# Kernel tuning notes

Hardware: AMD Instinct MI355X
Metric: run time of the kernel (lower is better)

The kernel has to match this reference:

```python
import jax, jax.numpy as jnp
import numpy as np

NB, H = 4, 16
EPS = 1e-5


def _ln(x, w=None, b=None):
    m = jnp.mean(x, -1, keepdims=True)
    v = jnp.var(x, -1, keepdims=True)
    y = (x - m) * jax.lax.rsqrt(v + EPS)
    if w is not None:
        y = y * w
    if b is not None:
        y = y + b
    return y


def _ada_ln(a, s, ln_s_w, w_gamma, w_beta):
    # AF3 Algorithm 26: a <- sigmoid(Lin(LN_nobias(s))) * LN_noaffine(a) + Lin(LN_nobias(s))
    a_n = _ln(a)
    s_n = _ln(s, ln_s_w)
    return jax.nn.sigmoid(s_n @ w_gamma) * a_n + s_n @ w_beta


def setup_inputs():
    key = jax.random.key(0)
    B, S, c_a, c_s, c_z = 1, 1024, 768, 384, 128
    n_hidden = 2 * c_a  # expansion factor n=2
    ks = iter(jax.random.split(key, 40))

    def rn(shape, scale=1.0):
        return scale * jax.random.normal(next(ks), shape, dtype=jnp.float32)

    p = 0.02
    return {
        "a": rn((B, S, c_a)),
        "s": rn((B, S, c_s)),
        "z": rn((B, S, S, c_z)),
        "beta": rn((B, S, S, H)),
        # per-block AttentionPairBias params (stacked over NB blocks)
        "ln_s_w_attn": jnp.ones((NB, c_s)),
        "wg_attn": rn((NB, c_s, c_a), p),
        "wb_attn": rn((NB, c_s, c_a), p),
        "wq": rn((NB, c_a, c_a), p),
        "bq": jnp.zeros((NB, c_a)),
        "wk": rn((NB, c_a, c_a), p),
        "wv": rn((NB, c_a, c_a), p),
        "ln_z_w": jnp.ones((NB, c_z)),
        "ln_z_b": jnp.zeros((NB, c_z)),
        "wpb": rn((NB, c_z, H), p),
        "wgate": rn((NB, c_a, c_a), p),
        "wo": rn((NB, c_a, c_a), p),
        "wsg_attn": rn((NB, c_s, c_a), p),
        "bsg_attn": -2.0 * jnp.ones((NB, c_a)),
        # per-block ConditionedTransitionBlock params
        "ln_s_w_tr": jnp.ones((NB, c_s)),
        "wg_tr": rn((NB, c_s, c_a), p),
        "wb_tr": rn((NB, c_s, c_a), p),
        "w_swish": rn((NB, c_a, n_hidden), p),
        "w_gate2": rn((NB, c_a, n_hidden), p),
        "wsg_tr": rn((NB, c_s, c_a), p),
        "bsg_tr": -2.0 * jnp.ones((NB, c_a)),
        "w_out": rn((NB, n_hidden, c_a), p),
    }


def reference(a, s, z, beta, ln_s_w_attn, wg_attn, wb_attn, wq, bq, wk, wv,
              ln_z_w, ln_z_b, wpb, wgate, wo, wsg_attn, bsg_attn,
              ln_s_w_tr, wg_tr, wb_tr, w_swish, w_gate2, wsg_tr, bsg_tr, w_out):
    B, S, c_a = a.shape
    d = c_a // H
    scale = 1.0 / jnp.sqrt(jnp.float32(d))
    for i in range(NB):
        # --- AttentionPairBias (AF3 Alg 24) ---
        ah = _ada_ln(a, s, ln_s_w_attn[i], wg_attn[i], wb_attn[i])
        q = (ah @ wq[i] + bq[i]).reshape(B, S, H, d)
        k = (ah @ wk[i]).reshape(B, S, H, d)
        v = (ah @ wv[i]).reshape(B, S, H, d)
        zb = _ln(z, ln_z_w[i], ln_z_b[i]) @ wpb[i]  # [B,S,S,H] pair bias
        scores = jnp.einsum('bihd,bjhd->bhij', q, k) * scale \
                 + jnp.transpose(zb + beta, (0, 3, 1, 2))
        attn = jax.nn.softmax(scores, axis=-1)
        o = jnp.einsum('bhij,bjhd->bihd', attn, v)
        g = jax.nn.sigmoid(ah @ wgate[i]).reshape(B, S, H, d)
        att_out = (g * o).reshape(B, S, c_a) @ wo[i]
        b_attn = jax.nn.sigmoid(s @ wsg_attn[i] + bsg_attn[i]) * att_out
        # --- ConditionedTransitionBlock (AF3 Alg 25, SwiGLU) ---
        th = _ada_ln(a, s, ln_s_w_tr[i], wg_tr[i], wb_tr[i])
        hidden = jax.nn.silu(th @ w_swish[i]) * (th @ w_gate2[i])
        tr = jax.nn.sigmoid(s @ wsg_tr[i] + bsg_tr[i]) * (hidden @ w_out[i])
        a = b_attn + tr
    return a
```

## Files before the change

kernel.cpp:

```cpp
#include <hip/hip_runtime.h>
#include <hip/hip_bf16.h>

typedef __hip_bfloat16 bf16;
typedef __attribute__((ext_vector_type(8))) short s8v;
typedef __attribute__((ext_vector_type(4))) float f4v;

constexpr int S = 1024, CA = 768, CS = 384, CZ = 128, NHID = 1536;
constexpr int NBLK = 4, NHEAD = 16, DH = 48;
constexpr float EPS = 1e-5f;

#define DEV static __device__ __forceinline__

DEV float sigmoidf_(float x) { return 1.0f / (1.0f + __expf(-x)); }

DEV f4v mfma16(s8v a, s8v b, f4v c) {
  return __builtin_amdgcn_mfma_f32_16x16x32_bf16(a, b, c, 0, 0, 0);
}

union U8 { s8v s; bf16 h[8]; };
union U4 { uint2 u; bf16 h[4]; };

DEV float wred_sum(float v) {
#pragma unroll
  for (int o = 32; o; o >>= 1) v += __shfl_xor(v, o);
  return v;
}

__global__ __launch_bounds__(256) void rowln_s(const float* __restrict__ x,
                                               bf16* __restrict__ s_hat,
                                               bf16* __restrict__ s_bf) {
  constexpr int C = CS, C4 = C / 4;
  __shared__ float red[8];
  const int t = threadIdx.x;
  const size_t row = blockIdx.x;
  float4 v = make_float4(0.f, 0.f, 0.f, 0.f);
  if (t < C4) v = ((const float4*)(x + row * C))[t];
  float sum = v.x + v.y + v.z + v.w;
  float sq = v.x * v.x + v.y * v.y + v.z * v.z + v.w * v.w;
  sum = wred_sum(sum); sq = wred_sum(sq);
  const int wv = t >> 6;
  if ((t & 63) == 0) { red[2 * wv] = sum; red[2 * wv + 1] = sq; }
  __syncthreads();
  sum = red[0] + red[2] + red[4] + red[6];
  sq = red[1] + red[3] + red[5] + red[7];
  const float m = sum / C;
  const float rstd = rsqrtf(sq / C - m * m + EPS);
  if (t < C4) {
    U4 oh, ob_;
    oh.h[0] = __float2bfloat16((v.x - m) * rstd); oh.h[1] = __float2bfloat16((v.y - m) * rstd);
    oh.h[2] = __float2bfloat16((v.z - m) * rstd); oh.h[3] = __float2bfloat16((v.w - m) * rstd);
    ob_.h[0] = __float2bfloat16(v.x); ob_.h[1] = __float2bfloat16(v.y);
    ob_.h[2] = __float2bfloat16(v.z); ob_.h[3] = __float2bfloat16(v.w);
    *(uint2*)(s_hat + row * C + 4 * t) = oh.u;
    *(uint2*)(s_bf + row * C + 4 * t) = ob_.u;
  }
}

__global__ __launch_bounds__(256) void ln_adaln2(const float* __restrict__ a,
                                                 const bf16* __restrict__ ada,
                                                 bf16* __restrict__ ah_attn,
                                                 bf16* __restrict__ ah_tr) {
  __shared__ float red[8];
  const int t = threadIdx.x;
  const size_t row = blockIdx.x;
  float4 v = make_float4(0.f, 0.f, 0.f, 0.f);
  if (t < 192) v = ((const float4*)(a + row * CA))[t];
  float sum = v.x + v.y + v.z + v.w;
  float sq = v.x * v.x + v.y * v.y + v.z * v.z + v.w * v.w;
  sum = wred_sum(sum); sq = wred_sum(sq);
  const int wv = t >> 6;
  if ((t & 63) == 0) { red[2 * wv] = sum; red[2 * wv + 1] = sq; }
  __syncthreads();
  sum = red[0] + red[2] + red[4] + red[6];
  sq = red[1] + red[3] + red[5] + red[7];
  const float m = sum / CA;
  const float rstd = rsqrtf(sq / CA - m * m + EPS);
  if (t < 192) {
    const float an[4] = {(v.x - m) * rstd, (v.y - m) * rstd, (v.z - m) * rstd, (v.w - m) * rstd};
    const bf16* ar = ada + row * 12288 + 4 * t;
    U4 g1, b1, g2, b2, o1, o2;
    g1.u = *(const uint2*)(ar);
    b1.u = *(const uint2*)(ar + 768);
    g2.u = *(const uint2*)(ar + 1536);
    b2.u = *(const uint2*)(ar + 2304);
#pragma unroll
    for (int j = 0; j < 4; ++j) {
      o1.h[j] = __float2bfloat16(sigmoidf_(__bfloat162float(g1.h[j])) * an[j] + __bfloat162float(b1.h[j]));
      o2.h[j] = __float2bfloat16(sigmoidf_(__bfloat162float(g2.h[j])) * an[j] + __bfloat162float(b2.h[j]));
    }
    *(uint2*)(ah_attn + row * CA + 4 * t) = o1.u;
    *(uint2*)(ah_tr + row * CA + 4 * t) = o2.u;
  }
}

__global__ __launch_bounds__(256) void final_adaln(const float* __restrict__ sg,
                                                   const bf16* __restrict__ att,
                                                   const bf16* __restrict__ tr,
                                                   const bf16* __restrict__ ada,
                                                   bf16* __restrict__ ah_attn,
                                                   bf16* __restrict__ ah_tr) {
  __shared__ float red[8];
  const int t = threadIdx.x;
  const size_t row = blockIdx.x;
  float o[4] = {0.f, 0.f, 0.f, 0.f};
  if (t < 192) {
    const float4 sa = *(const float4*)(sg + row * 6144 + 4 * t);
    const float4 st = *(const float4*)(sg + row * 6144 + 768 + 4 * t);
    U4 av, tv;
    av.u = *(const uint2*)(att + row * CA + 4 * t);
    tv.u = *(const uint2*)(tr + row * CA + 4 * t);
    o[0] = sa.x * __bfloat162float(av.h[0]) + st.x * __bfloat162float(tv.h[0]);
    o[1] = sa.y * __bfloat162float(av.h[1]) + st.y * __bfloat162float(tv.h[1]);
    o[2] = sa.z * __bfloat162float(av.h[2]) + st.z * __bfloat162float(tv.h[2]);
    o[3] = sa.w * __bfloat162float(av.h[3]) + st.w * __bfloat162float(tv.h[3]);
  }
  float sum = o[0] + o[1] + o[2] + o[3];
  float sq = o[0] * o[0] + o[1] * o[1] + o[2] * o[2] + o[3] * o[3];
  sum = wred_sum(sum); sq = wred_sum(sq);
  const int wv = t >> 6;
  if ((t & 63) == 0) { red[2 * wv] = sum; red[2 * wv + 1] = sq; }
  __syncthreads();
  sum = red[0] + red[2] + red[4] + red[6];
  sq = red[1] + red[3] + red[5] + red[7];
  const float m = sum / CA;
  const float rstd = rsqrtf(sq / CA - m * m + EPS);
  if (t < 192) {
    const bf16* ar = ada + row * 12288 + 4 * t;
    U4 g1, b1, g2, b2, o1, o2;
    g1.u = *(const uint2*)(ar);
    b1.u = *(const uint2*)(ar + 768);
    g2.u = *(const uint2*)(ar + 1536);
    b2.u = *(const uint2*)(ar + 2304);
#pragma unroll
    for (int j = 0; j < 4; ++j) {
      const float an = (o[j] - m) * rstd;
      o1.h[j] = __float2bfloat16(sigmoidf_(__bfloat162float(g1.h[j])) * an + __bfloat162float(b1.h[j]));
      o2.h[j] = __float2bfloat16(sigmoidf_(__bfloat162float(g2.h[j])) * an + __bfloat162float(b2.h[j]));
    }
    *(uint2*)(ah_attn + row * CA + 4 * t) = o1.u;
    *(uint2*)(ah_tr + row * CA + 4 * t) = o2.u;
  }
}

__global__ __launch_bounds__(256) void ew_final(const float* __restrict__ sg,
                                                const bf16* __restrict__ att,
                                                const bf16* __restrict__ tr,
                                                float* __restrict__ out) {
  const int i = blockIdx.x * 256 + threadIdx.x;
  const int row = i / 192, col = (i % 192) * 4;
  const float4 sa = *(const float4*)(sg + (size_t)row * 6144 + col);
  const float4 st = *(const float4*)(sg + (size_t)row * 6144 + 768 + col);
  U4 av, tv;
  av.u = *(const uint2*)(att + (size_t)row * CA + col);
  tv.u = *(const uint2*)(tr + (size_t)row * CA + col);
  float4 o;
  o.x = sa.x * __bfloat162float(av.h[0]) + st.x * __bfloat162float(tv.h[0]);
  o.y = sa.y * __bfloat162float(av.h[1]) + st.y * __bfloat162float(tv.h[1]);
  o.z = sa.z * __bfloat162float(av.h[2]) + st.z * __bfloat162float(tv.h[2]);
  o.w = sa.w * __bfloat162float(av.h[3]) + st.w * __bfloat162float(tv.h[3]);
  *(float4*)(out + (size_t)row * CA + col) = o;
}

struct TGroup {
  const float* src[6];
  bf16* dst[6];
  const float* cs[6];
  long dstZ[6];
};

__global__ __launch_bounds__(256) void transpose_grp(TGroup g, int K, int N, int csZ) {
  __shared__ float tile[32][33];
  const int z = blockIdx.z, wsel = z >> 2, blk = z & 3;
  const float* src = g.src[wsel] + (size_t)blk * K * N;
  bf16* dst = g.dst[wsel] + (size_t)blk * g.dstZ[wsel];
  const float* cs = g.cs[wsel];
  const int k0 = blockIdx.y * 32, n0 = blockIdx.x * 32;
  const int tx = threadIdx.x & 31, ty = threadIdx.x >> 5;
#pragma unroll
  for (int q = 0; q < 4; ++q) {
    const int k = k0 + ty + 8 * q;
    float v = src[(size_t)k * N + n0 + tx];
    if (cs) v *= cs[(size_t)blk * csZ + k];
    tile[ty + 8 * q][tx] = v;
  }
  __syncthreads();
#pragma unroll
  for (int q = 0; q < 4; ++q)
    dst[(size_t)(n0 + ty + 8 * q) * K + k0 + tx] = __float2bfloat16(tile[tx][ty + 8 * q]);
}

__global__ __launch_bounds__(256) void prep_all(const float* __restrict__ ln_z_w,
                                                const float* __restrict__ ln_z_b,
                                                const float* __restrict__ wpb,
                                                bf16* __restrict__ W2T,
                                                float* __restrict__ bias2,
                                                const float* __restrict__ bq,
                                                const float* __restrict__ bsg_attn,
                                                const float* __restrict__ bsg_tr,
                                                float* __restrict__ biasQKVG,
                                                float* __restrict__ biasSG) {
  const int blk = blockIdx.x;
  const int t = threadIdx.x;
  if (blk == 48) {
    for (int f = t; f < 64 * CZ; f += 256) {
      const int col = f >> 7, c = f & 127, b = col >> 4, h = col & 15;
      W2T[f] = __float2bfloat16(ln_z_w[b * CZ + c] * wpb[(b * CZ + c) * NHEAD + h]);
    }
    if (t < 64) {
      const int b = t >> 4, h = t & 15;
      float sum = 0.f;
      for (int c = 0; c < CZ; ++c)
        sum += ln_z_b[b * CZ + c] * wpb[(b * CZ + c) * NHEAD + h];
      bias2[t] = sum;
    }
    return;
  }
  const int g = blk * 256 + t;
  if (g < 4 * 3072) {
    const int b = g / 3072, c = g % 3072;
    biasQKVG[g] = (c < 768) ? bq[b * 768 + c] : 0.f;
  }
  if (g < 6144) {
    const int b = g / 1536, c = g % 1536;
    biasSG[g] = (c < 768) ? bsg_attn[b * 768 + c] : bsg_tr[b * 768 + c - 768];
  }
}

__global__ __launch_bounds__(256) void zbias_kernel(const float* __restrict__ z,
                                                    const float* __restrict__ beta,
                                                    const bf16* __restrict__ W2T,
                                                    const float* __restrict__ bias2,
                                                    bf16* __restrict__ bias_all) {
  __shared__ s8v zt8[64 * 16];
  __shared__ s8v w2s[64 * 16];
  __shared__ float betas[64][17];
  __shared__ float bias2s[64];
  __shared__ bf16 obuf[64][72];
  const int t = threadIdx.x;
  const int i = blockIdx.y, j0 = blockIdx.x * 64;
#pragma unroll
  for (int q = 0; q < 4; ++q) {
    const int u = q * 256 + t;
    const int row = u >> 4, sl = u & 15;
    w2s[row * 16 + (sl ^ (row & 7))] = *(const s8v*)(W2T + row * CZ + sl * 8);
  }
  if (t < 64) bias2s[t] = bias2[t];
  {
    const int j = t >> 2, h4 = t & 3;
    const float4 bv = *(const float4*)(beta + ((size_t)i * S + j0 + j) * NHEAD + 4 * h4);
    betas[j][4 * h4 + 0] = bv.x; betas[j][4 * h4 + 1] = bv.y;
    betas[j][4 * h4 + 2] = bv.z; betas[j][4 * h4 + 3] = bv.w;
  }
  {
    const int p = t >> 2, q = t & 3;
    const float* zr = z + ((size_t)i * S + j0 + p) * CZ + q * 32;
    float vals[32];
    float sum = 0.f, sq = 0.f;
#pragma unroll
    for (int k4 = 0; k4 < 8; ++k4) {
      const float4 xv = *(const float4*)(zr + 4 * k4);
      vals[4 * k4 + 0] = xv.x; vals[4 * k4 + 1] = xv.y;
      vals[4 * k4 + 2] = xv.z; vals[4 * k4 + 3] = xv.w;
      sum += xv.x + xv.y + xv.z + xv.w;
      sq += xv.x * xv.x + xv.y * xv.y + xv.z * xv.z + xv.w * xv.w;
    }
    sum += __shfl_xor(sum, 1); sum += __shfl_xor(sum, 2);
    sq += __shfl_xor(sq, 1); sq += __shfl_xor(sq, 2);
    const float m = sum / CZ;
    const float rstd = rsqrtf(sq / CZ - m * m + EPS);
#pragma unroll
    for (int u = 0; u < 4; ++u) {
      U8 pk;
#pragma unroll
      for (int e = 0; e < 8; ++e) pk.h[e] = __float2bfloat16((vals[8 * u + e] - m) * rstd);
      const int cu = 4 * q + u;
      zt8[p * 16 + (cu ^ (p & 7))] = pk.s;
    }
  }
  __syncthreads();
  const int lane = t & 63, wid = t >> 6;
  const int wr = wid >> 1, wc = wid & 1;
  const int ln = lane & 15, lq = lane >> 4;
  f4v acc[2][2] = {};
#pragma unroll
  for (int kk = 0; kk < 4; ++kk) {
    const int sl = (lq + 4 * kk) ^ (ln & 7);
    s8v a[2], b[2];
#pragma unroll
    for (int mi = 0; mi < 2; ++mi) a[mi] = zt8[(32 * wr + 16 * mi + ln) * 16 + sl];
#pragma unroll
    for (int ni = 0; ni < 2; ++ni) b[ni] = w2s[(32 * wc + 16 * ni + ln) * 16 + sl];
#pragma unroll
    for (int mi = 0; mi < 2; ++mi)
#pragma unroll
      for (int ni = 0; ni < 2; ++ni) acc[mi][ni] = mfma16(a[mi], b[ni], acc[mi][ni]);
  }
#pragma unroll
  for (int mi = 0; mi < 2; ++mi)
#pragma unroll
    for (int ni = 0; ni < 2; ++ni) {
      const int col = 32 * wc + 16 * ni + ln;
      const int jb = 32 * wr + 16 * mi + 4 * lq;
      U4 o4;
#pragma unroll
      for (int r = 0; r < 4; ++r)
        o4.h[r] = __float2bfloat16(acc[mi][ni][r] + bias2s[col] + betas[jb + r][col & 15]);
      *(uint2*)&obuf[col][jb] = o4.u;
    }
  __syncthreads();
  {
    const int oc = t >> 2, js = (t & 3) * 16;
    bf16* dp = bias_all + (size_t)oc * S * S + (size_t)i * S + j0 + js;
    *(s8v*)dp = *(const s8v*)&obuf[oc][js];
    *(s8v*)(dp + 8) = *(const s8v*)&obuf[oc][js + 8];
  }
}

struct GemmAArgs {
  const bf16* A0[2]; int lda0[2];
  const bf16* A1[2]; int lda1[2];
  const bf16* Bt[2];
  const float* bias[2];
  void* C[2];
  int K[2]; int N[2]; int nb[2];
  int amode[2]; int outMode[2];
  bf16* vT;
};

DEV s8v combineRT(s8v x, s8v y, int amode) {
  U8 ux, uy, rr;
  ux.s = x; uy.s = y;
#pragma unroll
  for (int j = 0; j < 8; ++j) {
    const float fx = __bfloat162float(ux.h[j]);
    const float fy = __bfloat162float(uy.h[j]);
    const float tt = sigmoidf_(fx);
    rr.h[j] = __float2bfloat16((amode == 2 ? fx * tt : tt) * fy);
  }
  return rr.s;
}

__global__ __launch_bounds__(256) void gemmA(GemmAArgs ga) {
  const int z = blockIdx.z;
  if ((int)blockIdx.x >= ga.nb[z]) return;
  __shared__ s8v As[512];
  __shared__ s8v Bs[1024];
  const bf16* A0 = ga.A0[z]; const int lda0 = ga.lda0[z];
  const bf16* A1 = ga.A1[z]; const int lda1 = ga.lda1[z];
  const bf16* Bt = ga.Bt[z];
  const float* bias = ga.bias[z];
  const int K = ga.K[z], N = ga.N[z], amode = ga.amode[z], om = ga.outMode[z];
  const int t = threadIdx.x;
  const int lane = t & 63, wid = t >> 6;
  const int wr = wid >> 1, wc = wid & 1;
  const int ln = lane & 15, lq = lane >> 4;
  const int m0 = blockIdx.y * 64, n0 = blockIdx.x * 128;
  int rowA[2], slA[2], swzA[2];
#pragma unroll
  for (int q = 0; q < 2; ++q) {
    const int u = q * 256 + t;
    rowA[q] = u >> 3; slA[q] = u & 7;
    swzA[q] = rowA[q] * 8 + (slA[q] ^ (rowA[q] & 7));
  }
  int rowB[4], slB[4], swzB[4];
#pragma unroll
  for (int q = 0; q < 4; ++q) {
    const int u = q * 256 + t;
    rowB[q] = u >> 3; slB[q] = u & 7;
    swzB[q] = rowB[q] * 8 + (slB[q] ^ (rowB[q] & 7));
  }
  f4v acc[2][4] = {};
  s8v ra[2], ra2[2], rb[4];
#pragma unroll
  for (int q = 0; q < 2; ++q) {
    ra[q] = *(const s8v*)(A0 + (size_t)(m0 + rowA[q]) * lda0 + slA[q] * 8);
    if (amode != 0) ra2[q] = *(const s8v*)(A1 + (size_t)(m0 + rowA[q]) * lda1 + slA[q] * 8);
  }
#pragma unroll
  for (int q = 0; q < 4; ++q)
    rb[q] = *(const s8v*)(Bt + (size_t)(n0 + rowB[q]) * K + slB[q] * 8);
  for (int ks = 0;;) {
    __syncthreads();
#pragma unroll
    for (int q = 0; q < 2; ++q)
      As[swzA[q]] = (amode == 0) ? ra[q] : combineRT(ra[q], ra2[q], amode);
#pragma unroll
    for (int q = 0; q < 4; ++q) Bs[swzB[q]] = rb[q];
    const int ksn = ks + 64;
    if (ksn < K) {
#pragma unroll
      for (int q = 0; q < 2; ++q) {
        ra[q] = *(const s8v*)(A0 + (size_t)(m0 + rowA[q]) * lda0 + ksn + slA[q] * 8);
        if (amode != 0) ra2[q] = *(const s8v*)(A1 + (size_t)(m0 + rowA[q]) * lda1 + ksn + slA[q] * 8);
      }
#pragma unroll
      for (int q = 0; q < 4; ++q)
        rb[q] = *(const s8v*)(Bt + (size_t)(n0 + rowB[q]) * K + ksn + slB[q] * 8);
    }
    __syncthreads();
#pragma unroll
    for (int kk = 0; kk < 2; ++kk) {
      const int sl = (lq + 4 * kk) ^ (ln & 7);
      s8v a[2], b[4];
#pragma unroll
      for (int mi = 0; mi < 2; ++mi) a[mi] = As[(32 * wr + 16 * mi + ln) * 8 + sl];
#pragma unroll
      for (int ni = 0; ni < 4; ++ni) b[ni] = Bs[(64 * wc + 16 * ni + ln) * 8 + sl];
#pragma unroll
      for (int mi = 0; mi < 2; ++mi)
#pragma unroll
        for (int ni = 0; ni < 4; ++ni) acc[mi][ni] = mfma16(a[mi], b[ni], acc[mi][ni]);
    }
    ks = ksn;
    if (ks >= K) break;
  }
  const bool vdiv = (ga.vT != nullptr) && (z == 0) && (n0 >= 1536) && (n0 < 2304);
#pragma unroll
  for (int ni = 0; ni < 4; ++ni) {
    const int n = n0 + 64 * wc + 16 * ni + ln;
    const float bv = bias ? bias[n] : 0.f;
#pragma unroll
    for (int mi = 0; mi < 2; ++mi) {
      const int mb = m0 + 32 * wr + 16 * mi + 4 * lq;
      if (vdiv) {
        U4 o4;
#pragma unroll
        for (int r = 0; r < 4; ++r) o4.h[r] = __float2bfloat16(acc[mi][ni][r] + bv);
        *(uint2*)(ga.vT + (size_t)(n - 1536) * S + mb) = o4.u;
      } else if (om == 0) {
        bf16* Cb = (bf16*)ga.C[z];
#pragma unroll
        for (int r = 0; r < 4; ++r)
          Cb[(size_t)(mb + r) * N + n] = __float2bfloat16(acc[mi][ni][r] + bv);
      } else {
        float* Cf = (float*)ga.C[z];
#pragma unroll
        for (int r = 0; r < 4; ++r)
          Cf[(size_t)(mb + r) * N + n] = sigmoidf_(acc[mi][ni][r] + bv);
      }
    }
  }
}

__global__ __launch_bounds__(256) void flash_split(const bf16* __restrict__ qkvg,
                                                   const bf16* __restrict__ vT,
                                                   const bf16* __restrict__ bias_all,
                                                   float* __restrict__ opart,
                                                   float* __restrict__ ml, int blk) {
  __shared__ s8v Qs[64 * 8];
  __shared__ s8v Ks[2][64 * 8];
  __shared__ s8v Vs[2][48 * 8];
  __shared__ s8v Bs[2][64 * 8];
  __shared__ bf16 PwB[4 * 1024];
  __shared__ float facL[4][16];
  const int t = threadIdx.x;
  const int lane = t & 63, w = t >> 6;
  const int ln = lane & 15, lq = lane >> 4;
  const int h = blockIdx.y, i0 = blockIdx.x * 64, half = blockIdx.z;
  const bf16* bp = bias_all + (size_t)(blk * NHEAD + h) * S * S;
  const float scale = 0.14433756729740643f;

#pragma unroll
  for (int uu = 0; uu < 2; ++uu) {
    const int u = t + 256 * uu, row = u >> 3, sl = u & 7;
    s8v qv{};
    if (sl < 6) qv = *(const s8v*)(qkvg + (size_t)(i0 + row) * 3072 + h * DH + sl * 8);
    Qs[row * 8 + (sl ^ (row & 7))] = qv;
  }

  s8v kr[2], br[2], vr0{}, vr1{};
  auto prefetch = [&](int jt) {
    const int j0 = jt * 64;
#pragma unroll
    for (int uu = 0; uu < 2; ++uu) {
      const int u = t + 256 * uu, row = u >> 3, sl = u & 7;
      s8v kv{};
      if (sl < 6) kv = *(const s8v*)(qkvg + (size_t)(j0 + row) * 3072 + 768 + h * DH + sl * 8);
      kr[uu] = kv;
      br[uu] = *(const s8v*)(bp + (size_t)(i0 + row) * S + j0 + sl * 8);
    }
    { const int d = t >> 3, sl = t & 7;
      vr0 = *(const s8v*)(vT + (size_t)(h * DH + d) * S + j0 + sl * 8); }
    if (t < 128) {
      const int u = 256 + t, d = u >> 3, sl = u & 7;
      vr1 = *(const s8v*)(vT + (size_t)(h * DH + d) * S + j0 + sl * 8);
    }
  };
  auto store_tiles = [&](int pb) {
#pragma unroll
    for (int uu = 0; uu < 2; ++uu) {
      const int u = t + 256 * uu, row = u >> 3, sl = u & 7;
      const int ph = row * 8 + (sl ^ (row & 7));
      Ks[pb][ph] = kr[uu];
      Bs[pb][ph] = br[uu];
    }
    { const int d = t >> 3, sl = t & 7;
      Vs[pb][d * 8 + (sl ^ (d & 7))] = vr0; }
    if (t < 128) {
      const int u = 256 + t, d = u >> 3, sl = u & 7;
      Vs[pb][d * 8 + (sl ^ (d & 7))] = vr1;
    }
  };

  float m_run = -3e30f, l_run = 0.f;
  f4v acc_o[3] = {};
  bf16* pw = PwB + w * 1024;

  prefetch(half * 8);
  for (int jt2 = 0; jt2 < 8; ++jt2) {
    const int pb = jt2 & 1;
    __syncthreads();
    store_tiles(pb);
    __syncthreads();
    if (jt2 < 7) prefetch(half * 8 + jt2 + 1);
    float p[4][4];
    float tmax = -3e30f;
#pragma unroll
    for (int ja = 0; ja < 4; ++ja) {
      f4v accs = {};
#pragma unroll
      for (int ks2 = 0; ks2 < 2; ++ks2) {
        const int sl = (lq + 4 * ks2) ^ (ln & 7);
        const s8v a = Ks[pb][(16 * ja + ln) * 8 + sl];
        const s8v b = Qs[(16 * w + ln) * 8 + sl];
        accs = mfma16(a, b, accs);
      }
      const int jq = 4 * ja + lq;
      const int pu = jq >> 1;
      U4 bv;
      bv.u = *(const uint2*)((const bf16*)(&Bs[pb][0]) +
                             (((16 * w + ln) * 8 + (pu ^ (ln & 7))) * 8 + (jq & 1) * 4));
#pragma unroll
      for (int r = 0; r < 4; ++r) {
        p[ja][r] = accs[r] * scale + __bfloat162float(bv.h[r]);
        tmax = fmaxf(tmax, p[ja][r]);
      }
    }
    tmax = fmaxf(tmax, __shfl_xor(tmax, 16));
    tmax = fmaxf(tmax, __shfl_xor(tmax, 32));
    const float m_new = fmaxf(m_run, tmax);
    const float fac = __expf(m_run - m_new);
    m_run = m_new;
    float psum = 0.f;
#pragma unroll
    for (int ja = 0; ja < 4; ++ja)
#pragma unroll
      for (int r = 0; r < 4; ++r) {
        p[ja][r] = __expf(p[ja][r] - m_new);
        psum += p[ja][r];
      }
    psum += __shfl_xor(psum, 16);
    psum += __shfl_xor(psum, 32);
    l_run = l_run * fac + psum;
    if (lq == 0) facL[w][ln] = fac;
#pragma unroll
    for (int ja = 0; ja < 4; ++ja) {
      const int ju = 4 * ja + lq;
      const int ph = ju ^ ((ln & 7) << 1);
      U4 pk;
#pragma unroll
      for (int r = 0; r < 4; ++r) pk.h[r] = __float2bfloat16(p[ja][r]);
      *(uint2*)(pw + ln * 64 + ph * 4) = pk.u;
    }
    asm volatile("s_waitcnt lgkmcnt(0)" ::: "memory");
    __builtin_amdgcn_sched_barrier(0);
    const float4 fv = *(const float4*)&facL[w][4 * lq];
#pragma unroll
    for (int ni = 0; ni < 3; ++ni) {
      acc_o[ni][0] *= fv.x; acc_o[ni][1] *= fv.y;
      acc_o[ni][2] *= fv.z; acc_o[ni][3] *= fv.w;
    }
#pragma unroll
    for (int ks2 = 0; ks2 < 2; ++ks2) {
      const int pu0 = (2 * lq + 8 * ks2) ^ ((ln & 7) << 1);
      const s8v pa = *(const s8v*)(pw + ln * 64 + pu0 * 4);
      const int slv = (lq + 4 * ks2) ^ (ln & 7);
#pragma unroll
      for (int ni = 0; ni < 3; ++ni) {
        const s8v vb = Vs[pb][(16 * ni + ln) * 8 + slv];
        acc_o[ni] = mfma16(pa, vb, acc_o[ni]);
      }
    }
  }
  if (lq == 0) {
    ((float2*)ml)[(size_t)(half * NHEAD + h) * S + i0 + 16 * w + ln] =
        make_float2(m_run, l_run);
  }
  float* op = opart + (size_t)half * S * CA;
#pragma unroll
  for (int ni = 0; ni < 3; ++ni)
#pragma unroll
    for (int r = 0; r < 4; ++r) {
      const int m = i0 + 16 * w + 4 * lq + r;
      op[(size_t)m * CA + h * DH + 16 * ni + ln] = acc_o[ni][r];
    }
}

__global__ __launch_bounds__(256) void flash_combine(const float* __restrict__ opart,
                                                     const float* __restrict__ ml,
                                                     bf16* __restrict__ ob) {
  const int row = blockIdx.x, t = threadIdx.x;
  if (t >= 192) return;
  const int c = 4 * t, h = t / 12;
  const float2 a = ((const float2*)ml)[(size_t)h * S + row];
  const float2 b = ((const float2*)ml)[(size_t)(NHEAD + h) * S + row];
  const float M = fmaxf(a.x, b.x);
  const float w1 = __expf(a.x - M), w2 = __expf(b.x - M);
  const float inv = 1.0f / (w1 * a.y + w2 * b.y);
  const float4 o1 = *(const float4*)(opart + (size_t)row * CA + c);
  const float4 o2 = *(const float4*)(opart + (size_t)S * CA + (size_t)row * CA + c);
  U4 o;
  o.h[0] = __float2bfloat16((w1 * o1.x + w2 * o2.x) * inv);
  o.h[1] = __float2bfloat16((w1 * o1.y + w2 * o2.y) * inv);
  o.h[2] = __float2bfloat16((w1 * o1.z + w2 * o2.z) * inv);
  o.h[3] = __float2bfloat16((w1 * o1.w + w2 * o2.w) * inv);
  *(uint2*)(ob + (size_t)row * CA + c) = o.u;
}

__global__ void fill_kernel(float* p, int n, float v) {
  const int i = blockIdx.x * 256 + threadIdx.x;
  if (i < n) p[i] = v;
}

extern "C" void kernel_launch(void* const* d_in, const int* in_sizes, int n_in,
                              void* d_out, int out_size, void* d_ws, size_t ws_size,
                              hipStream_t stream) {
  (void)in_sizes; (void)n_in;
  const float* a_in = (const float*)d_in[0];
  const float* s_in = (const float*)d_in[1];
  const float* z_in = (const float*)d_in[2];
  const float* beta = (const float*)d_in[3];
  const float* ln_s_w_attn = (const float*)d_in[4];
  const float* wg_attn = (const float*)d_in[5];
  const float* wb_attn = (const float*)d_in[6];
  const float* wq = (const float*)d_in[7];
  const float* bq = (const float*)d_in[8];
  const float* wk = (const float*)d_in[9];
  const float* wv = (const float*)d_in[10];
  const float* ln_z_w = (const float*)d_in[11];
  const float* ln_z_b = (const float*)d_in[12];
  const float* wpb = (const float*)d_in[13];
  const float* wgate = (const float*)d_in[14];
  const float* wo = (const float*)d_in[15];
  const float* wsg_attn = (const float*)d_in[16];
  const float* bsg_attn = (const float*)d_in[17];
  const float* ln_s_w_tr = (const float*)d_in[18];
  const float* wg_tr = (const float*)d_in[19];
  const float* wb_tr = (const float*)d_in[20];
  const float* w_swish = (const float*)d_in[21];
  const float* w_gate2 = (const float*)d_in[22];
  const float* wsg_tr = (const float*)d_in[23];
  const float* bsg_tr = (const float*)d_in[24];
  const float* w_out = (const float*)d_in[25];

  char* wp = (char*)d_ws;
  size_t used = 0;
  auto alloc = [&](size_t bytes) -> void* {
    void* p = wp + used;
    used += (bytes + 255) & ~(size_t)255;
    return p;
  };
  bf16* bias_all = (bf16*)alloc((size_t)64 * S * S * 2);
  bf16* WT_ada = (bf16*)alloc((size_t)4 * 3072 * 384 * 2);
  bf16* WT_sg = (bf16*)alloc((size_t)4 * 1536 * 384 * 2);
  bf16* WT_qkvg = (bf16*)alloc((size_t)4 * 3072 * 768 * 2);
  bf16* WT_wo = (bf16*)alloc((size_t)4 * 768 * 768 * 2);
  bf16* WT_mlp = (bf16*)alloc((size_t)4 * 3072 * 768 * 2);
  bf16* WT_wout = (bf16*)alloc((size_t)4 * 768 * 1536 * 2);
  float* biasQKVG = (float*)alloc(4 * 3072 * 4);
  float* biasSG = (float*)alloc(6144 * 4);
  bf16* W2T = (bf16*)alloc(64 * 128 * 2);
  float* bias2 = (float*)alloc(64 * 4);
  bf16* ada_all = (bf16*)alloc((size_t)S * 12288 * 2);
  float* sg_all = (float*)alloc((size_t)S * 6144 * 4);
  bf16* s_hat = (bf16*)alloc((size_t)S * CS * 2);
  bf16* s_bf = (bf16*)alloc((size_t)S * CS * 2);
  bf16* ah_attn = (bf16*)alloc((size_t)S * CA * 2);
  bf16* ah_tr = (bf16*)alloc((size_t)S * CA * 2);
  bf16* qkvg = (bf16*)alloc((size_t)S * 3072 * 2);
  bf16* vT = (bf16*)alloc((size_t)CA * S * 2);
  bf16* ob = (bf16*)alloc((size_t)S * CA * 2);
  bf16* att = (bf16*)alloc((size_t)S * CA * 2);
  bf16* swg = (bf16*)alloc((size_t)S * 3072 * 2);
  bf16* trout = (bf16*)alloc((size_t)S * CA * 2);
  float* opart = (float*)alloc((size_t)2 * S * CA * 4);
  float* ml = (float*)alloc((size_t)2 * NHEAD * S * 8);
  if (used > ws_size) {
    fill_kernel<<<(out_size + 255) / 256, 256, 0, stream>>>((float*)d_out, out_size, 12345.0f);
    return;
  }

  const dim3 B256(256);

  prep_all<<<49, B256, 0, stream>>>(ln_z_w, ln_z_b, wpb, W2T, bias2,
                                    bq, bsg_attn, bsg_tr, biasQKVG, biasSG);

  {
    TGroup g{};
    g.src[0] = wg_attn;  g.dst[0] = WT_ada + (size_t)0 * 384;    g.cs[0] = ln_s_w_attn; g.dstZ[0] = 3072 * 384;
    g.src[1] = wb_attn;  g.dst[1] = WT_ada + (size_t)768 * 384;  g.cs[1] = ln_s_w_attn; g.dstZ[1] = 3072 * 384;
    g.src[2] = wg_tr;    g.dst[2] = WT_ada + (size_t)1536 * 384; g.cs[2] = ln_s_w_tr;   g.dstZ[2] = 3072 * 384;
    g.src[3] = wb_tr;    g.dst[3] = WT_ada + (size_t)2304 * 384; g.cs[3] = ln_s_w_tr;   g.dstZ[3] = 3072 * 384;
    g.src[4] = wsg_attn; g.dst[4] = WT_sg + (size_t)0 * 384;     g.cs[4] = nullptr;     g.dstZ[4] = 1536 * 384;
    g.src[5] = wsg_tr;   g.dst[5] = WT_sg + (size_t)768 * 384;   g.cs[5] = nullptr;     g.dstZ[5] = 1536 * 384;
    transpose_grp<<<dim3(24, 12, 24), B256, 0, stream>>>(g, 384, 768, CS);
  }
  {
    TGroup g{};
    g.src[0] = wq;    g.dst[0] = WT_qkvg + (size_t)0 * 768;    g.dstZ[0] = 3072 * 768;
    g.src[1] = wk;    g.dst[1] = WT_qkvg + (size_t)768 * 768;  g.dstZ[1] = 3072 * 768;
    g.src[2] = wv;    g.dst[2] = WT_qkvg + (size_t)1536 * 768; g.dstZ[2] = 3072 * 768;
    g.src[3] = wgate; g.dst[3] = WT_qkvg + (size_t)2304 * 768; g.dstZ[3] = 3072 * 768;
    g.src[4] = wo;    g.dst[4] = WT_wo;                        g.dstZ[4] = 768 * 768;
    transpose_grp<<<dim3(24, 24, 20), B256, 0, stream>>>(g, 768, 768, 0);
  }
  {
    TGroup g{};
    g.src[0] = w_swish; g.dst[0] = WT_mlp + (size_t)0 * 768;    g.dstZ[0] = 3072 * 768;
    g.src[1] = w_gate2; g.dst[1] = WT_mlp + (size_t)1536 * 768; g.dstZ[1] = 3072 * 768;
    transpose_grp<<<dim3(48, 24, 8), B256, 0, stream>>>(g, 768, 1536, 0);
  }
  {
    TGroup g{};
    g.src[0] = w_out; g.dst[0] = WT_wout; g.dstZ[0] = 768 * 1536;
    transpose_grp<<<dim3(24, 48, 4), B256, 0, stream>>>(g, 1536, 768, 0);
  }

  rowln_s<<<S, B256, 0, stream>>>(s_in, s_hat, s_bf);
  zbias_kernel<<<dim3(16, 1024), B256, 0, stream>>>(z_in, beta, W2T, bias2, bias_all);

  {
    GemmAArgs ga{};
    ga.A0[0] = s_hat; ga.lda0[0] = 384; ga.Bt[0] = WT_ada; ga.bias[0] = nullptr;
    ga.C[0] = ada_all; ga.K[0] = 384; ga.N[0] = 12288; ga.nb[0] = 96;
    ga.amode[0] = 0; ga.outMode[0] = 0;
    ga.A0[1] = s_bf; ga.lda0[1] = 384; ga.Bt[1] = WT_sg; ga.bias[1] = biasSG;
    ga.C[1] = sg_all; ga.K[1] = 384; ga.N[1] = 6144; ga.nb[1] = 48;
    ga.amode[1] = 0; ga.outMode[1] = 1;
    ga.vT = nullptr;
    gemmA<<<dim3(96, 16, 2), B256, 0, stream>>>(ga);
  }

  ln_adaln2<<<S, B256, 0, stream>>>(a_in, ada_all, ah_attn, ah_tr);
  for (int b = 0; b < NBLK; ++b) {
    {
      GemmAArgs ga{};
      ga.A0[0] = ah_attn; ga.lda0[0] = 768; ga.Bt[0] = WT_qkvg + (size_t)b * 3072 * 768;
      ga.bias[0] = biasQKVG + b * 3072; ga.C[0] = qkvg; ga.K[0] = 768; ga.N[0] = 3072;
      ga.nb[0] = 24; ga.amode[0] = 0; ga.outMode[0] = 0;
      ga.A0[1] = ah_tr; ga.lda0[1] = 768; ga.Bt[1] = WT_mlp + (size_t)b * 3072 * 768;
      ga.bias[1] = nullptr; ga.C[1] = swg; ga.K[1] = 768; ga.N[1] = 3072;
      ga.nb[1] = 24; ga.amode[1] = 0; ga.outMode[1] = 0;
      ga.vT = vT;
      gemmA<<<dim3(24, 16, 2), B256, 0, stream>>>(ga);
    }
    flash_split<<<dim3(16, 16, 2), B256, 0, stream>>>(qkvg, vT, bias_all, opart, ml, b);
    flash_combine<<<S, B256, 0, stream>>>(opart, ml, ob);
    {
      GemmAArgs ga{};
      ga.A0[0] = qkvg + 2304; ga.lda0[0] = 3072; ga.A1[0] = ob; ga.lda1[0] = 768;
      ga.Bt[0] = WT_wo + (size_t)b * 768 * 768; ga.bias[0] = nullptr;
      ga.C[0] = att; ga.K[0] = 768; ga.N[0] = 768; ga.nb[0] = 6;
      ga.amode[0] = 1; ga.outMode[0] = 0;
      ga.A0[1] = swg; ga.lda0[1] = 3072; ga.A1[1] = swg + 1536; ga.lda1[1] = 3072;
      ga.Bt[1] = WT_wout + (size_t)b * 768 * 1536; ga.bias[1] = nullptr;
      ga.C[1] = trout; ga.K[1] = 1536; ga.N[1] = 768; ga.nb[1] = 6;
      ga.amode[1] = 2; ga.outMode[1] = 0;
      ga.vT = nullptr;
      gemmA<<<dim3(6, 16, 2), B256, 0, stream>>>(ga);
    }
    if (b < NBLK - 1) {
      final_adaln<<<S, B256, 0, stream>>>(sg_all + (size_t)b * 1536, att, trout,
                                          ada_all + (size_t)(b + 1) * 3072, ah_attn, ah_tr);
    } else {
      ew_final<<<768, B256, 0, stream>>>(sg_all + (size_t)b * 1536, att, trout, (float*)d_out);
    }
  }
}
```

Measured before the change: 571.7 us.

## Merge prep kernels, split flash attention 4-way, fuse gate into combine

All weight transposes, bias prep and the s layernorm now run in one large launch, replacing six separate kernels. Flash attention splits keys into four parts instead of two, so more blocks run at once, and drops LDS double buffering. It also raises wave priority around the MFMA sections. The combine kernel merges four partials and applies the sigmoid gate, so the output GEMM reads a plain A operand. The trade-offs are larger partial buffers, more combine traffic, and lost overlap from single buffering.

New measurement: 581.5 us. Within noise of the previous version (+1.7%).

```diff
diff --git a/kernel.cpp b/kernel.cpp
--- a/kernel.cpp
+++ b/kernel.cpp
@@ -26,33 +26,102 @@
   return v;
 }
 
-__global__ __launch_bounds__(256) void rowln_s(const float* __restrict__ x,
-                                               bf16* __restrict__ s_hat,
-                                               bf16* __restrict__ s_bf) {
-  constexpr int C = CS, C4 = C / 4;
-  __shared__ float red[8];
-  const int t = threadIdx.x;
-  const size_t row = blockIdx.x;
-  float4 v = make_float4(0.f, 0.f, 0.f, 0.f);
-  if (t < C4) v = ((const float4*)(x + row * C))[t];
-  float sum = v.x + v.y + v.z + v.w;
-  float sq = v.x * v.x + v.y * v.y + v.z * v.z + v.w * v.w;
-  sum = wred_sum(sum); sq = wred_sum(sq);
-  const int wv = t >> 6;
-  if ((t & 63) == 0) { red[2 * wv] = sum; red[2 * wv + 1] = sq; }
-  __syncthreads();
-  sum = red[0] + red[2] + red[4] + red[6];
-  sq = red[1] + red[3] + red[5] + red[7];
-  const float m = sum / C;
-  const float rstd = rsqrtf(sq / C - m * m + EPS);
-  if (t < C4) {
-    U4 oh, ob_;
-    oh.h[0] = __float2bfloat16((v.x - m) * rstd); oh.h[1] = __float2bfloat16((v.y - m) * rstd);
-    oh.h[2] = __float2bfloat16((v.z - m) * rstd); oh.h[3] = __float2bfloat16((v.w - m) * rstd);
-    ob_.h[0] = __float2bfloat16(v.x); ob_.h[1] = __float2bfloat16(v.y);
-    ob_.h[2] = __float2bfloat16(v.z); ob_.h[3] = __float2bfloat16(v.w);
-    *(uint2*)(s_hat + row * C + 4 * t) = oh.u;
-    *(uint2*)(s_bf + row * C + 4 * t) = ob_.u;
+struct PrepFatArgs {
+  const float* tsrc[14];
+  bf16* tdst[14];
+  const float* tcs[14];
+  long tdstZ[14];
+  const float *ln_z_w, *ln_z_b, *wpb, *bq, *bsg_a, *bsg_t;
+  bf16* W2T; float* bias2; float* biasQKVG; float* biasSG;
+  const float* s_in; bf16* s_hat; bf16* s_bf;
+};
+
+__global__ __launch_bounds__(256) void prep_fat(PrepFatArgs a) {
+  __shared__ __align__(16) float tile[1056];
+  const int bid = blockIdx.x, t = threadIdx.x;
+  if (bid < 32256) {
+    int ti, blk, x, y, K, N;
+    if (bid < 6912) {
+      const int lb = bid; ti = lb / 1152; const int r2 = lb % 1152;
+      blk = r2 / 288; const int rem = r2 % 288; x = rem % 24; y = rem / 24; K = 384; N = 768;
+    } else if (bid < 18432) {
+      const int lb = bid - 6912; ti = 6 + lb / 2304; const int r2 = lb % 2304;
+      blk = r2 / 576; const int rem = r2 % 576; x = rem % 24; y = rem / 24; K = 768; N = 768;
+    } else if (bid < 27648) {
+      const int lb = bid - 18432; ti = 11 + lb / 4608; const int r2 = lb % 4608;
+      blk = r2 / 1152; const int rem = r2 % 1152; x = rem % 48; y = rem / 48; K = 768; N = 1536;
+    } else {
+      const int lb = bid - 27648; ti = 13; blk = lb / 1152;
+      const int rem = lb % 1152; x = rem % 24; y = rem / 24; K = 1536; N = 768;
+    }
+    const float* src = a.tsrc[ti] + (size_t)blk * K * N;
+    bf16* dst = a.tdst[ti] + (size_t)blk * a.tdstZ[ti];
+    const float* cs = a.tcs[ti] ? (a.tcs[ti] + blk * CS) : nullptr;
+    const int k0 = y * 32, n0 = x * 32, tx = t & 31, ty = t >> 5;
+#pragma unroll
+    for (int q = 0; q < 4; ++q) {
+      const int k = k0 + ty + 8 * q;
+      float v = src[(size_t)k * N + n0 + tx];
+      if (cs) v *= cs[k];
+      tile[(ty + 8 * q) * 33 + tx] = v;
+    }
+    __syncthreads();
+#pragma unroll
+    for (int q = 0; q < 4; ++q)
+      dst[(size_t)(n0 + ty + 8 * q) * K + k0 + tx] = __float2bfloat16(tile[tx * 33 + ty + 8 * q]);
+    return;
+  }
+  if (bid < 32305) {
+    const int pid = bid - 32256;
+    if (pid == 48) {
+      for (int f = t; f < 64 * CZ; f += 256) {
+        const int col = f >> 7, c = f & 127, b = col >> 4, h = col & 15;
+        a.W2T[f] = __float2bfloat16(a.ln_z_w[b * CZ + c] * a.wpb[(b * CZ + c) * NHEAD + h]);
+      }
+      if (t < 64) {
+        const int b = t >> 4, h = t & 15;
+        float sum = 0.f;
+        for (int c = 0; c < CZ; ++c)
+          sum += a.ln_z_b[b * CZ + c] * a.wpb[(b * CZ + c) * NHEAD + h];
+        a.bias2[t] = sum;
+      }
+      return;
+    }
+    const int g = pid * 256 + t;
+    if (g < 4 * 3072) {
+      const int b = g / 3072, c = g % 3072;
+      a.biasQKVG[g] = (c < 768) ? a.bq[b * 768 + c] : 0.f;
+    }
+    if (g < 6144) {
+      const int b = g / 1536, c = g % 1536;
+      a.biasSG[g] = (c < 768) ? a.bsg_a[b * 768 + c] : a.bsg_t[b * 768 + c - 768];
+    }
+    return;
+  }
+  {
+    float* red = tile;
+    const size_t row = bid - 32305;
+    float4 v = make_float4(0.f, 0.f, 0.f, 0.f);
+    if (t < CS / 4) v = ((const float4*)(a.s_in + row * CS))[t];
+    float sum = v.x + v.y + v.z + v.w;
+    float sq = v.x * v.x + v.y * v.y + v.z * v.z + v.w * v.w;
+    sum = wred_sum(sum); sq = wred_sum(sq);
+    const int wv = t >> 6;
+    if ((t & 63) == 0) { red[2 * wv] = sum; red[2 * wv + 1] = sq; }
+    __syncthreads();
+    sum = red[0] + red[2] + red[4] + red[6];
+    sq = red[1] + red[3] + red[5] + red[7];
+    const float m = sum / CS;
+    const float rstd = rsqrtf(sq / CS - m * m + EPS);
+    if (t < CS / 4) {
+      U4 oh, ob_;
+      oh.h[0] = __float2bfloat16((v.x - m) * rstd); oh.h[1] = __float2bfloat16((v.y - m) * rstd);
+      oh.h[2] = __float2bfloat16((v.z - m) * rstd); oh.h[3] = __float2bfloat16((v.w - m) * rstd);
+      ob_.h[0] = __float2bfloat16(v.x); ob_.h[1] = __float2bfloat16(v.y);
+      ob_.h[2] = __float2bfloat16(v.z); ob_.h[3] = __float2bfloat16(v.w);
+      *(uint2*)(a.s_hat + row * CS + 4 * t) = oh.u;
+      *(uint2*)(a.s_bf + row * CS + 4 * t) = ob_.u;
+    }
   }
 }
 
@@ -161,71 +230,6 @@
   *(float4*)(out + (size_t)row * CA + col) = o;
 }
 
-struct TGroup {
-  const float* src[6];
-  bf16* dst[6];
-  const float* cs[6];
-  long dstZ[6];
-};
-
-__global__ __launch_bounds__(256) void transpose_grp(TGroup g, int K, int N, int csZ) {
-  __shared__ float tile[32][33];
-  const int z = blockIdx.z, wsel = z >> 2, blk = z & 3;
-  const float* src = g.src[wsel] + (size_t)blk * K * N;
-  bf16* dst = g.dst[wsel] + (size_t)blk * g.dstZ[wsel];
-  const float* cs = g.cs[wsel];
-  const int k0 = blockIdx.y * 32, n0 = blockIdx.x * 32;
-  const int tx = threadIdx.x & 31, ty = threadIdx.x >> 5;
-#pragma unroll
-  for (int q = 0; q < 4; ++q) {
-    const int k = k0 + ty + 8 * q;
-    float v = src[(size_t)k * N + n0 + tx];
-    if (cs) v *= cs[(size_t)blk * csZ + k];
-    tile[ty + 8 * q][tx] = v;
-  }
-  __syncthreads();
-#pragma unroll
-  for (int q = 0; q < 4; ++q)
-    dst[(size_t)(n0 + ty + 8 * q) * K + k0 + tx] = __float2bfloat16(tile[tx][ty + 8 * q]);
-}
-
-__global__ __launch_bounds__(256) void prep_all(const float* __restrict__ ln_z_w,
-                                                const float* __restrict__ ln_z_b,
-                                                const float* __restrict__ wpb,
-                                                bf16* __restrict__ W2T,
-                                                float* __restrict__ bias2,
-                                                const float* __restrict__ bq,
-                                                const float* __restrict__ bsg_attn,
-                                                const float* __restrict__ bsg_tr,
-                                                float* __restrict__ biasQKVG,
-                                                float* __restrict__ biasSG) {
-  const int blk = blockIdx.x;
-  const int t = threadIdx.x;
-  if (blk == 48) {
-    for (int f = t; f < 64 * CZ; f += 256) {
-      const int col = f >> 7, c = f & 127, b = col >> 4, h = col & 15;
-      W2T[f] = __float2bfloat16(ln_z_w[b * CZ + c] * wpb[(b * CZ + c) * NHEAD + h]);
-    }
-    if (t < 64) {
-      const int b = t >> 4, h = t & 15;
-      float sum = 0.f;
-      for (int c = 0; c < CZ; ++c)
-        sum += ln_z_b[b * CZ + c] * wpb[(b * CZ + c) * NHEAD + h];
-      bias2[t] = sum;
-    }
-    return;
-  }
-  const int g = blk * 256 + t;
-  if (g < 4 * 3072) {
-    const int b = g / 3072, c = g % 3072;
-    biasQKVG[g] = (c < 768) ? bq[b * 768 + c] : 0.f;
-  }
-  if (g < 6144) {
-    const int b = g / 1536, c = g % 1536;
-    biasSG[g] = (c < 768) ? bsg_attn[b * 768 + c] : bsg_tr[b * 768 + c - 768];
-  }
-}
-
 __global__ __launch_bounds__(256) void zbias_kernel(const float* __restrict__ z,
                                                     const float* __restrict__ beta,
                                                     const bf16* __restrict__ W2T,
@@ -448,15 +452,15 @@
                                                    float* __restrict__ opart,
                                                    float* __restrict__ ml, int blk) {
   __shared__ s8v Qs[64 * 8];
-  __shared__ s8v Ks[2][64 * 8];
-  __shared__ s8v Vs[2][48 * 8];
-  __shared__ s8v Bs[2][64 * 8];
+  __shared__ s8v Ks[64 * 8];
+  __shared__ s8v Vs[48 * 8];
+  __shared__ s8v Bs[64 * 8];
   __shared__ bf16 PwB[4 * 1024];
   __shared__ float facL[4][16];
   const int t = threadIdx.x;
   const int lane = t & 63, w = t >> 6;
   const int ln = lane & 15, lq = lane >> 4;
-  const int h = blockIdx.y, i0 = blockIdx.x * 64, half = blockIdx.z;
+  const int h = blockIdx.y, i0 = blockIdx.x * 64, part = blockIdx.z;
   const bf16* bp = bias_all + (size_t)(blk * NHEAD + h) * S * S;
   const float scale = 0.14433756729740643f;
 
@@ -486,19 +490,19 @@
       vr1 = *(const s8v*)(vT + (size_t)(h * DH + d) * S + j0 + sl * 8);
     }
   };
-  auto store_tiles = [&](int pb) {
+  auto store_tiles = [&]() {
 #pragma unroll
     for (int uu = 0; uu < 2; ++uu) {
       const int u = t + 256 * uu, row = u >> 3, sl = u & 7;
       const int ph = row * 8 + (sl ^ (row & 7));
-      Ks[pb][ph] = kr[uu];
-      Bs[pb][ph] = br[uu];
+      Ks[ph] = kr[uu];
+      Bs[ph] = br[uu];
     }
     { const int d = t >> 3, sl = t & 7;
-      Vs[pb][d * 8 + (sl ^ (d & 7))] = vr0; }
+      Vs[d * 8 + (sl ^ (d & 7))] = vr0; }
     if (t < 128) {
       const int u = 256 + t, d = u >> 3, sl = u & 7;
-      Vs[pb][d * 8 + (sl ^ (d & 7))] = vr1;
+      Vs[d * 8 + (sl ^ (d & 7))] = vr1;
     }
   };
 
@@ -506,29 +510,29 @@
   f4v acc_o[3] = {};
   bf16* pw = PwB + w * 1024;
 
-  prefetch(half * 8);
-  for (int jt2 = 0; jt2 < 8; ++jt2) {
-    const int pb = jt2 & 1;
+  prefetch(part * 4);
+  for (int jt2 = 0; jt2 < 4; ++jt2) {
     __syncthreads();
-    store_tiles(pb);
+    store_tiles();
     __syncthreads();
-    if (jt2 < 7) prefetch(half * 8 + jt2 + 1);
+    if (jt2 < 3) prefetch(part * 4 + jt2 + 1);
     float p[4][4];
     float tmax = -3e30f;
+    __builtin_amdgcn_s_setprio(1);
 #pragma unroll
     for (int ja = 0; ja < 4; ++ja) {
       f4v accs = {};
 #pragma unroll
       for (int ks2 = 0; ks2 < 2; ++ks2) {
         const int sl = (lq + 4 * ks2) ^ (ln & 7);
-        const s8v a = Ks[pb][(16 * ja + ln) * 8 + sl];
+        const s8v a = Ks[(16 * ja + ln) * 8 + sl];
         const s8v b = Qs[(16 * w + ln) * 8 + sl];
         accs = mfma16(a, b, accs);
       }
       const int jq = 4 * ja + lq;
       const int pu = jq >> 1;
       U4 bv;
-      bv.u = *(const uint2*)((const bf16*)(&Bs[pb][0]) +
+      bv.u = *(const uint2*)((const bf16*)(&Bs[0]) +
                              (((16 * w + ln) * 8 + (pu ^ (ln & 7))) * 8 + (jq & 1) * 4));
 #pragma unroll
       for (int r = 0; r < 4; ++r) {
@@ -536,6 +540,7 @@
         tmax = fmaxf(tmax, p[ja][r]);
       }
     }
+    __builtin_amdgcn_s_setprio(0);
     tmax = fmaxf(tmax, __shfl_xor(tmax, 16));
     tmax = fmaxf(tmax, __shfl_xor(tmax, 32));
     const float m_new = fmaxf(m_run, tmax);
@@ -570,6 +575,7 @@
       acc_o[ni][0] *= fv.x; acc_o[ni][1] *= fv.y;
       acc_o[ni][2] *= fv.z; acc_o[ni][3] *= fv.w;
     }
+    __builtin_amdgcn_s_setprio(1);
 #pragma unroll
     for (int ks2 = 0; ks2 < 2; ++ks2) {
       const int pu0 = (2 * lq + 8 * ks2) ^ ((ln & 7) << 1);
@@ -577,16 +583,17 @@
       const int slv = (lq + 4 * ks2) ^ (ln & 7);
 #pragma unroll
       for (int ni = 0; ni < 3; ++ni) {
-        const s8v vb = Vs[pb][(16 * ni + ln) * 8 + slv];
+        const s8v vb = Vs[(16 * ni + ln) * 8 + slv];
         acc_o[ni] = mfma16(pa, vb, acc_o[ni]);
       }
     }
+    __builtin_amdgcn_s_setprio(0);
   }
   if (lq == 0) {
-    ((float2*)ml)[(size_t)(half * NHEAD + h) * S + i0 + 16 * w + ln] =
+    ((float2*)ml)[(size_t)(part * NHEAD + h) * S + i0 + 16 * w + ln] =
         make_float2(m_run, l_run);
   }
-  float* op = opart + (size_t)half * S * CA;
+  float* op = opart + (size_t)part * S * CA;
 #pragma unroll
   for (int ni = 0; ni < 3; ++ni)
 #pragma unroll
@@ -596,25 +603,39 @@
     }
 }
 
-__global__ __launch_bounds__(256) void flash_combine(const float* __restrict__ opart,
-                                                     const float* __restrict__ ml,
-                                                     bf16* __restrict__ ob) {
+__global__ __launch_bounds__(256) void flash_combine4(const float* __restrict__ opart,
+                                                      const float* __restrict__ ml,
+                                                      const bf16* __restrict__ gate,
+                                                      bf16* __restrict__ go) {
   const int row = blockIdx.x, t = threadIdx.x;
   if (t >= 192) return;
   const int c = 4 * t, h = t / 12;
-  const float2 a = ((const float2*)ml)[(size_t)h * S + row];
-  const float2 b = ((const float2*)ml)[(size_t)(NHEAD + h) * S + row];
-  const float M = fmaxf(a.x, b.x);
-  const float w1 = __expf(a.x - M), w2 = __expf(b.x - M);
-  const float inv = 1.0f / (w1 * a.y + w2 * b.y);
-  const float4 o1 = *(const float4*)(opart + (size_t)row * CA + c);
-  const float4 o2 = *(const float4*)(opart + (size_t)S * CA + (size_t)row * CA + c);
+  const float2* mlp = (const float2*)ml;
+  const float2 a0 = mlp[(size_t)(0 * NHEAD + h) * S + row];
+  const float2 a1 = mlp[(size_t)(1 * NHEAD + h) * S + row];
+  const float2 a2 = mlp[(size_t)(2 * NHEAD + h) * S + row];
+  const float2 a3 = mlp[(size_t)(3 * NHEAD + h) * S + row];
+  const float M = fmaxf(fmaxf(a0.x, a1.x), fmaxf(a2.x, a3.x));
+  const float w0 = __expf(a0.x - M), w1 = __expf(a1.x - M);
+  const float w2 = __expf(a2.x - M), w3 = __expf(a3.x - M);
+  const float inv = 1.0f / (w0 * a0.y + w1 * a1.y + w2 * a2.y + w3 * a3.y);
+  const size_t rc = (size_t)row * CA + c;
+  const float4 o0 = *(const float4*)(opart + rc);
+  const float4 o1 = *(const float4*)(opart + (size_t)S * CA + rc);
+  const float4 o2 = *(const float4*)(opart + (size_t)2 * S * CA + rc);
+  const float4 o3 = *(const float4*)(opart + (size_t)3 * S * CA + rc);
+  U4 g;
+  g.u = *(const uint2*)(gate + (size_t)row * 3072 + c);
   U4 o;
-  o.h[0] = __float2bfloat16((w1 * o1.x + w2 * o2.x) * inv);
-  o.h[1] = __float2bfloat16((w1 * o1.y + w2 * o2.y) * inv);
-  o.h[2] = __float2bfloat16((w1 * o1.z + w2 * o2.z) * inv);
-  o.h[3] = __float2bfloat16((w1 * o1.w + w2 * o2.w) * inv);
-  *(uint2*)(ob + (size_t)row * CA + c) = o.u;
+  o.h[0] = __float2bfloat16(sigmoidf_(__bfloat162float(g.h[0])) *
+                            ((w0 * o0.x + w1 * o1.x + w2 * o2.x + w3 * o3.x) * inv));
+  o.h[1] = __float2bfloat16(sigmoidf_(__bfloat162float(g.h[1])) *
+                            ((w0 * o0.y + w1 * o1.y + w2 * o2.y + w3 * o3.y) * inv));
+  o.h[2] = __float2bfloat16(sigmoidf_(__bfloat162float(g.h[2])) *
+                            ((w0 * o0.z + w1 * o1.z + w2 * o2.z + w3 * o3.z) * inv));
+  o.h[3] = __float2bfloat16(sigmoidf_(__bfloat162float(g.h[3])) *
+                            ((w0 * o0.w + w1 * o1.w + w2 * o2.w + w3 * o3.w) * inv));
+  *(uint2*)(go + (size_t)row * CA + c) = o.u;
 }
 
 __global__ void fill_kernel(float* p, int n, float v) {
@@ -679,12 +700,12 @@
   bf16* ah_tr = (bf16*)alloc((size_t)S * CA * 2);
   bf16* qkvg = (bf16*)alloc((size_t)S * 3072 * 2);
   bf16* vT = (bf16*)alloc((size_t)CA * S * 2);
-  bf16* ob = (bf16*)alloc((size_t)S * CA * 2);
+  bf16* go = (bf16*)alloc((size_t)S * CA * 2);
   bf16* att = (bf16*)alloc((size_t)S * CA * 2);
   bf16* swg = (bf16*)alloc((size_t)S * 3072 * 2);
   bf16* trout = (bf16*)alloc((size_t)S * CA * 2);
-  float* opart = (float*)alloc((size_t)2 * S * CA * 4);
-  float* ml = (float*)alloc((size_t)2 * NHEAD * S * 8);
+  float* opart = (float*)alloc((size_t)4 * S * CA * 4);
+  float* ml = (float*)alloc((size_t)4 * NHEAD * S * 8);
   if (used > ws_size) {
     fill_kernel<<<(out_size + 255) / 256, 256, 0, stream>>>((float*)d_out, out_size, 12345.0f);
     return;
@@ -692,41 +713,29 @@
 
   const dim3 B256(256);
 
-  prep_all<<<49, B256, 0, stream>>>(ln_z_w, ln_z_b, wpb, W2T, bias2,
-                                    bq, bsg_attn, bsg_tr, biasQKVG, biasSG);
-
   {
-    TGroup g{};
-    g.src[0] = wg_attn;  g.dst[0] = WT_ada + (size_t)0 * 384;    g.cs[0] = ln_s_w_attn; g.dstZ[0] = 3072 * 384;
-    g.src[1] = wb_attn;  g.dst[1] = WT_ada + (size_t)768 * 384;  g.cs[1] = ln_s_w_attn; g.dstZ[1] = 3072 * 384;
-    g.src[2] = wg_tr;    g.dst[2] = WT_ada + (size_t)1536 * 384; g.cs[2] = ln_s_w_tr;   g.dstZ[2] = 3072 * 384;
-    g.src[3] = wb_tr;    g.dst[3] = WT_ada + (size_t)2304 * 384; g.cs[3] = ln_s_w_tr;   g.dstZ[3] = 3072 * 384;
-    g.src[4] = wsg_attn; g.dst[4] = WT_sg + (size_t)0 * 384;     g.cs[4] = nullptr;     g.dstZ[4] = 1536 * 384;
-    g.src[5] = wsg_tr;   g.dst[5] = WT_sg + (size_t)768 * 384;   g.cs[5] = nullptr;     g.dstZ[5] = 1536 * 384;
-    transpose_grp<<<dim3(24, 12, 24), B256, 0, stream>>>(g, 384, 768, CS);
-  }
-  {
-    TGroup g{};
-    g.src[0] = wq;    g.dst[0] = WT_qkvg + (size_t)0 * 768;    g.dstZ[0] = 3072 * 768;
-    g.src[1] = wk;    g.dst[1] = WT_qkvg + (size_t)768 * 768;  g.dstZ[1] = 3072 * 768;
-    g.src[2] = wv;    g.dst[2] = WT_qkvg + (size_t)1536 * 768; g.dstZ[2] = 3072 * 768;
-    g.src[3] = wgate; g.dst[3] = WT_qkvg + (size_t)2304 * 768; g.dstZ[3] = 3072 * 768;
-    g.src[4] = wo;    g.dst[4] = WT_wo;                        g.dstZ[4] = 768 * 768;
-    transpose_grp<<<dim3(24, 24, 20), B256, 0, stream>>>(g, 768, 768, 0);
-  }
-  {
-    TGroup g{};
-    g.src[0] = w_swish; g.dst[0] = WT_mlp + (size_t)0 * 768;    g.dstZ[0] = 3072 * 768;
-    g.src[1] = w_gate2; g.dst[1] = WT_mlp + (size_t)1536 * 768; g.dstZ[1] = 3072 * 768;
-    transpose_grp<<<dim3(48, 24, 8), B256, 0, stream>>>(g, 768, 1536, 0);
-  }
-  {
-    TGroup g{};
-    g.src[0] = w_out; g.dst[0] = WT_wout; g.dstZ[0] = 768 * 1536;
-    transpose_grp<<<dim3(24, 48, 4), B256, 0, stream>>>(g, 1536, 768, 0);
-  }
-
-  rowln_s<<<S, B256, 0, stream>>>(s_in, s_hat, s_bf);
+    PrepFatArgs pa{};
+    pa.tsrc[0] = wg_attn;  pa.tdst[0] = WT_ada + (size_t)0 * 384;    pa.tcs[0] = ln_s_w_attn; pa.tdstZ[0] = 3072 * 384;
+    pa.tsrc[1] = wb_attn;  pa.tdst[1] = WT_ada + (size_t)768 * 384;  pa.tcs[1] = ln_s_w_attn; pa.tdstZ[1] = 3072 * 384;
+    pa.tsrc[2] = wg_tr;    pa.tdst[2] = WT_ada + (size_t)1536 * 384; pa.tcs[2] = ln_s_w_tr;   pa.tdstZ[2] = 3072 * 384;
+    pa.tsrc[3] = wb_tr;    pa.tdst[3] = WT_ada + (size_t)2304 * 384; pa.tcs[3] = ln_s_w_tr;   pa.tdstZ[3] = 3072 * 384;
+    pa.tsrc[4] = wsg_attn; pa.tdst[4] = WT_sg + (size_t)0 * 384;     pa.tcs[4] = nullptr;     pa.tdstZ[4] = 1536 * 384;
+    pa.tsrc[5] = wsg_tr;   pa.tdst[5] = WT_sg + (size_t)768 * 384;   pa.tcs[5] = nullptr;     pa.tdstZ[5] = 1536 * 384;
+    pa.tsrc[6] = wq;    pa.tdst[6] = WT_qkvg + (size_t)0 * 768;    pa.tdstZ[6] = 3072 * 768;
+    pa.tsrc[7] = wk;    pa.tdst[7] = WT_qkvg + (size_t)768 * 768;  pa.tdstZ[7] = 3072 * 768;
+    pa.tsrc[8] = wv;    pa.tdst[8] = WT_qkvg + (size_t)1536 * 768; pa.tdstZ[8] = 3072 * 768;
+    pa.tsrc[9] = wgate; pa.tdst[9] = WT_qkvg + (size_t)2304 * 768; pa.tdstZ[9] = 3072 * 768;
+    pa.tsrc[10] = wo;   pa.tdst[10] = WT_wo;                       pa.tdstZ[10] = 768 * 768;
+    pa.tsrc[11] = w_swish; pa.tdst[11] = WT_mlp + (size_t)0 * 768;    pa.tdstZ[11] = 3072 * 768;
+    pa.tsrc[12] = w_gate2; pa.tdst[12] = WT_mlp + (size_t)1536 * 768; pa.tdstZ[12] = 3072 * 768;
+    pa.tsrc[13] = w_out; pa.tdst[13] = WT_wout; pa.tdstZ[13] = 768 * 1536;
+    pa.ln_z_w = ln_z_w; pa.ln_z_b = ln_z_b; pa.wpb = wpb;
+    pa.bq = bq; pa.bsg_a = bsg_attn; pa.bsg_t = bsg_tr;
+    pa.W2T = W2T; pa.bias2 = bias2; pa.biasQKVG = biasQKVG; pa.biasSG = biasSG;
+    pa.s_in = s_in; pa.s_hat = s_hat; pa.s_bf = s_bf;
+    prep_fat<<<33329, B256, 0, stream>>>(pa);
+  }
+
   zbias_kernel<<<dim3(16, 1024), B256, 0, stream>>>(z_in, beta, W2T, bias2, bias_all);
 
   {
@@ -754,14 +763,14 @@
       ga.vT = vT;
       gemmA<<<dim3(24, 16, 2), B256, 0, stream>>>(ga);
     }
-    flash_split<<<dim3(16, 16, 2), B256, 0, stream>>>(qkvg, vT, bias_all, opart, ml, b);
-    flash_combine<<<S, B256, 0, stream>>>(opart, ml, ob);
+    flash_split<<<dim3(16, 16, 4), B256, 0, stream>>>(qkvg, vT, bias_all, opart, ml, b);
+    flash_combine4<<<S, B256, 0, stream>>>(opart, ml, qkvg + 2304, go);
     {
       GemmAArgs ga{};
-      ga.A0[0] = qkvg + 2304; ga.lda0[0] = 3072; ga.A1[0] = ob; ga.lda1[0] = 768;
+      ga.A0[0] = go; ga.lda0[0] = 768;
       ga.Bt[0] = WT_wo + (size_t)b * 768 * 768; ga.bias[0] = nullptr;
       ga.C[0] = att; ga.K[0] = 768; ga.N[0] = 768; ga.nb[0] = 6;
-      ga.amode[0] = 1; ga.outMode[0] = 0;
+      ga.amode[0] = 0; ga.outMode[0] = 0;
       ga.A0[1] = swg; ga.lda0[1] = 3072; ga.A1[1] = swg + 1536; ga.lda1[1] = 3072;
       ga.Bt[1] = WT_wout + (size_t)b * 768 * 1536; ga.bias[1] = nullptr;
       ga.C[1] = trout; ga.K[1] = 1536; ga.N[1] = 768; ga.nb[1] = 6;
```
